# Kernel optimization log

Hardware: AMD Instinct MI355X
Metric: run time of the kernel (lower is better)

The kernel has to match this reference:

```python
import jax, jax.numpy as jnp
import numpy as np

D, H, W = 40, 32, 88
BEV_H, BEV_W = 125, 125
X_MIN, X_MAX, DX = -50.0, 50.0, 0.8
Y_MIN, Y_MAX, DY = -50.0, 50.0, 0.8
Z_MIN, DZ = -10.0, 20.0


def _voxel_indices():
    """Replicates frustum creation + get_geometry + index computation.
    Returns (flat_idx, valid) each of shape (D, H, W). Faithful to the
    original's sequential in-place max() semantics."""
    # depth_grid = arange(1, 41, 1) + 1  -> 2..41
    depth = jnp.arange(1.0, 41.0, 1.0) + 1.0            # (D,)
    xs = jnp.linspace(0.0, W - 1.0, W)                  # (W,)
    ys = jnp.linspace(0.0, H - 1.0, H)                  # (H,)
    d = depth[:, None, None]                            # (D,1,1)
    xd = jnp.broadcast_to(xs[None, None, :] * d, (D, H, W))  # x*depth
    yd = jnp.broadcast_to(ys[None, :, None] * d, (D, H, W))  # y*depth
    zd = jnp.broadcast_to(d, (D, H, W))                       # depth
    # first points_d.max(): over columns (xd, yd, zd)
    max1 = jnp.maximum(xd.max(), jnp.maximum(yd.max(), zd.max()))
    gx = xd / max1 * (X_MAX - X_MIN) + X_MIN
    # second points_d.max(): column 0 was overwritten in-place by gx
    max2 = jnp.maximum(gx.max(), jnp.maximum(yd.max(), zd.max()))
    gy = yd / max2 * (Y_MAX - Y_MIN) + Y_MIN
    gz = zd
    # voxelize (torch .long() truncates; all values here are >= 0)
    ix = ((gx - X_MIN) / DX).astype(jnp.int32)
    iy = ((gy - Y_MIN) / DY).astype(jnp.int32)
    iz = ((gz - Z_MIN) / DZ).astype(jnp.int32)
    valid = (ix >= 0) & (ix < BEV_W) & (iy >= 0) & (iy < BEV_H) & (iz >= 0)
    flat_idx = jnp.where(valid, iy * BEV_W + ix, 0)
    return flat_idx, valid


def setup_inputs() -> dict:
    key = jax.random.key(0)
    k1, k2, k3, k4, k5 = jax.random.split(key, 5)
    B, N, C = 1, 6, 128
    return {
        "img_feat": jax.random.normal(k1, (B, N, C, H, W), dtype=jnp.float32),
        "depth_logits": jax.random.normal(k2, (B, N, D, H, W), dtype=jnp.float32),
        "rots": jax.random.normal(k3, (B, N, 3, 3), dtype=jnp.float32),
        "trans": jax.random.normal(k4, (B, N, 3), dtype=jnp.float32),
        "intrins": jax.random.normal(k5, (B, N, 3, 3), dtype=jnp.float32),
    }


def reference(img_feat, depth_logits, rots, trans, intrins):
    B, N, C, h, w = img_feat.shape
    depth_probs = jax.nn.softmax(depth_logits, axis=2)         # (B,N,D,H,W)
    # depth-weighted outer product: (B,N,D,H,W,C)
    feats = jnp.einsum('bnchw,bndhw->bndhwc', img_feat, depth_probs)
    flat_feats = feats.reshape(-1, C)                          # (B*N*D*H*W, C)
    flat_idx, valid = _voxel_indices()                         # (D,H,W)
    idx = jnp.broadcast_to(flat_idx[None, None], (B, N, D, h, w)).reshape(-1)
    msk = jnp.broadcast_to(valid[None, None], (B, N, D, h, w)).reshape(-1)
    flat_feats = jnp.where(msk[:, None], flat_feats, 0.0)
    bev = jax.ops.segment_sum(flat_feats, idx, num_segments=BEV_H * BEV_W)
    bev = bev.reshape(BEV_H, BEV_W, C)
    return jnp.transpose(bev, (2, 0, 1))[None]                 # (1, C, 125, 125)
```

## Files before the change

kernel.cpp:

```cpp
#include <hip/hip_runtime.h>


constexpr int D = 40, H = 32, W = 88, HW = H * W;
constexpr int C = 128, NCAM = 6;
constexpr int BEV = 125, NBINS = BEV * BEV;
constexpr int NCOLS = NCAM * HW;
constexpr int LISTCAP = 192;

typedef __attribute__((ext_vector_type(8))) unsigned short us8;
typedef __attribute__((ext_vector_type(4))) float f4;

__device__ __forceinline__ unsigned short f2bf(float x) {
    unsigned u = __float_as_uint(x);
    return (unsigned short)((u + 0x7FFF + ((u >> 16) & 1)) >> 16);
}
__device__ __forceinline__ float b2f(unsigned short u) {
    return __uint_as_float(((unsigned)u) << 16);
}

struct Tabs { short XP[D][126]; short YP[D][126]; };
constexpr Tabs make_tabs() {
    Tabs t{};
    for (int d = 0; d < D; ++d) {
        int dep = d + 2;
        int cntx[126] = {};
        for (int w = 0; w < W; ++w) {
            float gx = (float)(w * dep) / 3567.0f * 100.0f - 50.0f;
            int ix = (int)((gx + 50.0f) / 0.8f);
            if (ix < 125) cntx[ix]++;
        }
        t.XP[d][0] = 0;
        for (int X = 0; X < 125; ++X) t.XP[d][X + 1] = (short)(t.XP[d][X] + cntx[X]);
        int cnty[126] = {};
        for (int h = 0; h < H; ++h) {
            float gy = (float)(h * dep) / 1271.0f * 100.0f - 50.0f;
            int iy = (int)((gy + 50.0f) / 0.8f);
            if (iy < 125) cnty[iy]++;
        }
        t.YP[d][0] = 0;
        for (int Y = 0; Y < 125; ++Y) t.YP[d][Y + 1] = (short)(t.YP[d][Y] + cnty[Y]);
    }
    return t;
}
__device__ const Tabs g_tab = make_tabs();

struct SegTable { unsigned a[4096]; unsigned b[4096]; int n; };

constexpr SegTable make_segs() {
    SegTable S{};
    Tabs t = make_tabs();
    int ns = 0;
    for (int iy = 0; iy < 125; ++iy) {
        int cnt[125] = {};
        for (int d = 0; d < D; ++d) {
            int yc = t.YP[d][iy + 1] - t.YP[d][iy];
            if (yc == 0) continue;
            for (int X = 0; X < 125; ++X)
                cnt[X] += (t.XP[d][X + 1] - t.XP[d][X]) * yc;
        }
        int X = 0;
        while (X < 125) {
            if (cnt[X] > 176) {
                int d0 = 0;
                while (d0 < D) {
                    int run = 0, d1 = d0;
                    while (d1 < D) {
                        int piece = (t.XP[d1][X + 1] - t.XP[d1][X]) *
                                    (t.YP[d1][iy + 1] - t.YP[d1][iy]);
                        if (d1 > d0 && run + piece > 128) break;
                        run += piece; ++d1;
                    }
                    if (run > 0) {
                        S.a[ns] = ((unsigned)iy << 16) | ((unsigned)X << 8) | (unsigned)(X + 1);
                        S.b[ns] = (1u << 31) | ((unsigned)d0 << 25) | ((unsigned)d1 << 19) | (unsigned)run;
                        ++ns;
                    }
                    d0 = d1;
                }
                ++X;
            } else {
                int X0 = X, run = 0;
                while (X < 125 && (X - X0) < 16 && cnt[X] <= 176 &&
                       (X == X0 || run + cnt[X] <= 128)) {
                    run += cnt[X]; ++X;
                }
                if (run > 0) {
                    S.a[ns] = ((unsigned)iy << 16) | ((unsigned)X0 << 8) | (unsigned)X;
                    S.b[ns] = ((unsigned)0 << 25) | ((unsigned)D << 19) | (unsigned)run;
                    ++ns;
                }
            }
        }
    }
    S.n = ns;
    return S;
}
constexpr SegTable g_ct = make_segs();
constexpr int NSEG = g_ct.n;
static_assert(NSEG > 0 && NSEG <= 4096, "seg table overflow");
__device__ const SegTable g_segs = g_ct;

constexpr int PACK_BLOCKS = (C / 8) * (HW / 32);
constexpr int SMAX_BLOCKS = NCOLS / 256;
constexpr int ZERO_TOTAL  = C * NBINS / 4;
constexpr int ZERO_BLOCKS = (ZERO_TOTAL + 1023) / 1024;
constexpr int MEGA_BLOCKS = PACK_BLOCKS + SMAX_BLOCKS + ZERO_BLOCKS;

__global__ void __launch_bounds__(256) mega_kernel(
        const float* __restrict__ feat,
        const float* __restrict__ logits,
        float* __restrict__ probs_t,
        unsigned short* __restrict__ feat_p,
        float* __restrict__ out) {
    __shared__ __align__(16) float tile[NCAM * 8 * 37];
    int b = blockIdx.x, t = threadIdx.x;

    if (b < PACK_BLOCKS) {
        int c0  = (b / 88) * 8;
        int hw0 = (b % 88) * 32;
        int cq = t >> 5, hwL = t & 31;
#pragma unroll
        for (int n = 0; n < NCAM; ++n)
            tile[(n * 8 + cq) * 37 + hwL] =
                feat[((size_t)(n * C + c0 + cq)) * HW + hw0 + hwL];
        __syncthreads();
        int hl = t >> 3, cL = t & 7;
        us8 v;
#pragma unroll
        for (int n = 0; n < NCAM; ++n)
            v[n] = f2bf(tile[(n * 8 + cL) * 37 + hl]);
        v[6] = 0; v[7] = 0;
        *(us8*)(feat_p + ((size_t)(hw0 + hl) * C + (c0 + cL)) * 8) = v;

    } else if (b < PACK_BLOCKS + SMAX_BLOCKS) {
        int col = (b - PACK_BLOCKS) * 256 + t;
        int n  = col / HW;
        int hw = col - n * HW;
        const float* src = logits + ((size_t)n * D) * HW + hw;
        float v[D];
        float m = -3.402823466e+38f;
#pragma unroll
        for (int d = 0; d < D; ++d) {
            v[d] = src[(size_t)d * HW];
            m = fmaxf(m, v[d]);
        }
        float s = 0.f;
#pragma unroll
        for (int d = 0; d < D; ++d) { v[d] = expf(v[d] - m); s += v[d]; }
        float inv = 1.0f / s;
#pragma unroll
        for (int d = 0; d < D; ++d)
            probs_t[(size_t)((d << 12) | hw) * 8 + n] = v[d] * inv;

    } else {
        int base = (b - PACK_BLOCKS - SMAX_BLOCKS) * 1024;
#pragma unroll
        for (int k = 0; k < 4; ++k) {
            int i = base + k * 256 + t;
            if (i < ZERO_TOTAL) ((f4*)out)[i] = f4{0.f, 0.f, 0.f, 0.f};
        }
    }
}

__global__ void __launch_bounds__(128, 8) gather_kernel(
        const unsigned short* __restrict__ feat_p,
        const float* __restrict__ probs_t,
        float* __restrict__ out) {
    __shared__ float T[2][16][66];
    __shared__ unsigned list[LISTCAP];
    int slot  = blockIdx.x >> 1;
    int chalf = blockIdx.x & 1;
    unsigned da = g_segs.a[slot], db = g_segs.b[slot];
    int iy = da >> 16, X0 = (da >> 8) & 0xFF, X1 = da & 0xFF;
    int width = X1 - X0;
    bool split = (db >> 31) != 0;
    int d0 = (db >> 25) & 0x3F, d1 = (db >> 19) & 0x3F;
    int P  = (int)(db & 0x7FFFF);
    int t = threadIdx.x;

    if (t < 64) {
        int d = d0 + t;
        if (d < d1) {
            int off = 0;
            for (int dd = d0; dd < d; ++dd)
                off += (g_tab.YP[dd][iy + 1] - g_tab.YP[dd][iy]) *
                       (g_tab.XP[dd][X1] - g_tab.XP[dd][X0]);
            int hb = g_tab.YP[d][iy], he = g_tab.YP[d][iy + 1];
            int p = off;
            for (int bl = 0; bl < width; ++bl) {
                int wb = g_tab.XP[d][X0 + bl], we = g_tab.XP[d][X0 + bl + 1];
                for (int h = hb; h < he; ++h)
                    for (int w = wb; w < we; ++w)
                        list[p++] = ((unsigned)bl << 18) | ((unsigned)d << 12)
                                  | (unsigned)(h * W + w);
            }
        }
    } else {
        float* Tf = &T[0][0][0];
        for (int i = t - 64; i < 2 * 16 * 66; i += 64) Tf[i] = 0.f;
    }
    __syncthreads();

    int lane = t & 63, dg = t >> 6;
    int c = chalf * 64 + lane;
    float* Tp = &T[dg][0][0];

    int npts = (P - dg + 1) >> 1;
    float racc = 0.f;
    int rbl = -1;
    for (int kb = 0; kb < npts; kb += 64) {
        int kidx = kb + lane;
        int myent = (int)list[min(dg + 2 * kidx, LISTCAP - 1)];
        int kk64 = min(64, npts - kb);
        for (int k0 = 0; k0 < kk64; k0 += 4) {
            int kk = min(4, kk64 - k0);
            unsigned pk[4]; us8 fv[4]; f4 pa[4], pb[4];
#pragma unroll
            for (int j = 0; j < 4; ++j) if (j < kk) {
                pk[j] = (unsigned)__shfl(myent, k0 + j);
                unsigned hw = pk[j] & 0xFFFu;
                fv[j] = *(const us8*)(feat_p + ((size_t)hw * C + (unsigned)c) * 8);
                const float* pp = probs_t + ((size_t)(pk[j] & 0x3FFFFu) << 3);
                pa[j] = *(const f4*)pp;
                pb[j] = *(const f4*)(pp + 4);
            }
#pragma unroll
            for (int j = 0; j < 4; ++j) if (j < kk) {
                float s = pa[j].x * b2f(fv[j][0]) + pa[j].y * b2f(fv[j][1])
                        + pa[j].z * b2f(fv[j][2]) + pa[j].w * b2f(fv[j][3])
                        + pb[j].x * b2f(fv[j][4]) + pb[j].y * b2f(fv[j][5]);
                int bl = (int)(pk[j] >> 18);
                if (bl != rbl) {
                    if (rbl >= 0) Tp[rbl * 66 + lane] += racc;
                    rbl = bl; racc = s;
                } else {
                    racc += s;
                }
            }
        }
    }
    if (rbl >= 0) Tp[rbl * 66 + lane] += racc;
    __syncthreads();

    int binbase = iy * BEV + X0;
#pragma unroll
    for (int it = 0; it < 8; ++it) {
        int bl = t & 15, cc = it * 8 + (t >> 4);
        if (bl < width) {
            float v = T[0][bl][cc] + T[1][bl][cc];
            float* dst = &out[(size_t)(chalf * 64 + cc) * NBINS + binbase + bl];
            if (split) atomicAdd(dst, v);
            else       *dst = v;
        }
    }
}

extern "C" void kernel_launch(void* const* d_in, const int* in_sizes, int n_in,
                              void* d_out, int out_size, void* d_ws, size_t ws_size,
                              hipStream_t stream) {
    const float* img_feat     = (const float*)d_in[0];
    const float* depth_logits = (const float*)d_in[1];
    float* out = (float*)d_out;

    char* p = (char*)d_ws;
    float*          probs_t = (float*)p;          p += (size_t)D * 4096 * 8 * 4;
    unsigned short* feat_p  = (unsigned short*)p; p += (size_t)HW * C * 8 * 2;

    mega_kernel<<<MEGA_BLOCKS, 256, 0, stream>>>(
        img_feat, depth_logits, probs_t, feat_p, out);
    gather_kernel<<<NSEG * 2, 128, 0, stream>>>(feat_p, probs_t, out);
}
```

Baseline: 125.4 us.

## Software-pipeline gather loads, prefetch list entries, and schedule heavy segments first

Replaces the batch-of-4 load-then-compute loop in the gather kernel with a double-buffered pipeline of three-entry groups. The next group's feature and probability loads are issued before the current group is consumed, and the next window's list entry is prefetched. Segments with large point counts are moved to the front of the table so long blocks start early and load imbalance at the tail shrinks. The launch bound drops from 8 to 4 waves per SIMD to leave registers for the extra buffers, at the cost of lower occupancy.

```diff
diff --git a/kernel.cpp b/kernel.cpp
--- a/kernel.cpp
+++ b/kernel.cpp
@@ -95,7 +95,19 @@
     S.n = ns;
     return S;
 }
-constexpr SegTable g_ct = make_segs();
+constexpr SegTable g_raw = make_segs();
+
+constexpr SegTable reorder_segs() {
+    SegTable R{};
+    int pos = 0;
+    for (int i = 0; i < g_raw.n; ++i)
+        if ((int)(g_raw.b[i] & 0x7FFFF) >= 120) { R.a[pos] = g_raw.a[i]; R.b[pos] = g_raw.b[i]; ++pos; }
+    for (int i = 0; i < g_raw.n; ++i)
+        if ((int)(g_raw.b[i] & 0x7FFFF) <  120) { R.a[pos] = g_raw.a[i]; R.b[pos] = g_raw.b[i]; ++pos; }
+    R.n = pos;
+    return R;
+}
+constexpr SegTable g_ct = reorder_segs();
 constexpr int NSEG = g_ct.n;
 static_assert(NSEG > 0 && NSEG <= 4096, "seg table overflow");
 __device__ const SegTable g_segs = g_ct;
@@ -162,7 +174,7 @@
     }
 }
 
-__global__ void __launch_bounds__(128, 8) gather_kernel(
+__global__ void __launch_bounds__(128, 4) gather_kernel(
         const unsigned short* __restrict__ feat_p,
         const float* __restrict__ probs_t,
         float* __restrict__ out) {
@@ -208,39 +220,54 @@
     int npts = (P - dg + 1) >> 1;
     float racc = 0.f;
     int rbl = -1;
+
+#define FETCH(I, BUF, P_)                                                     \
+    { pk##BUF[I] = (unsigned)__shfl(myent, (P_));                             \
+      fv##BUF[I] = *(const us8*)(feat_p +                                     \
+                    (((size_t)(pk##BUF[I] & 0xFFFu) * C + (unsigned)c) * 8)); \
+      const float* pp_ = probs_t + ((size_t)(pk##BUF[I] & 0x3FFFFu) << 3);    \
+      pa##BUF[I] = *(const f4*)pp_; pb##BUF[I] = *(const f4*)(pp_ + 4); }
+#define CONSUME(I, BUF)                                                       \
+    { float s_ = pa##BUF[I].x * b2f(fv##BUF[I][0]) + pa##BUF[I].y * b2f(fv##BUF[I][1]) \
+               + pa##BUF[I].z * b2f(fv##BUF[I][2]) + pa##BUF[I].w * b2f(fv##BUF[I][3]) \
+               + pb##BUF[I].x * b2f(fv##BUF[I][4]) + pb##BUF[I].y * b2f(fv##BUF[I][5]);\
+      int bl_ = (int)(pk##BUF[I] >> 18);                                      \
+      if (bl_ != rbl) { if (rbl >= 0) Tp[rbl * 66 + lane] += racc;            \
+                        rbl = bl_; racc = s_; }                               \
+      else racc += s_; }
+
+    int li0 = min(dg + 2 * lane, LISTCAP - 1);
+    int myent_next = (int)list[li0];
     for (int kb = 0; kb < npts; kb += 64) {
-        int kidx = kb + lane;
-        int myent = (int)list[min(dg + 2 * kidx, LISTCAP - 1)];
-        int kk64 = min(64, npts - kb);
-        for (int k0 = 0; k0 < kk64; k0 += 4) {
-            int kk = min(4, kk64 - k0);
-            unsigned pk[4]; us8 fv[4]; f4 pa[4], pb[4];
-#pragma unroll
-            for (int j = 0; j < 4; ++j) if (j < kk) {
-                pk[j] = (unsigned)__shfl(myent, k0 + j);
-                unsigned hw = pk[j] & 0xFFFu;
-                fv[j] = *(const us8*)(feat_p + ((size_t)hw * C + (unsigned)c) * 8);
-                const float* pp = probs_t + ((size_t)(pk[j] & 0x3FFFFu) << 3);
-                pa[j] = *(const f4*)pp;
-                pb[j] = *(const f4*)(pp + 4);
-            }
-#pragma unroll
-            for (int j = 0; j < 4; ++j) if (j < kk) {
-                float s = pa[j].x * b2f(fv[j][0]) + pa[j].y * b2f(fv[j][1])
-                        + pa[j].z * b2f(fv[j][2]) + pa[j].w * b2f(fv[j][3])
-                        + pb[j].x * b2f(fv[j][4]) + pb[j].y * b2f(fv[j][5]);
-                int bl = (int)(pk[j] >> 18);
-                if (bl != rbl) {
-                    if (rbl >= 0) Tp[rbl * 66 + lane] += racc;
-                    rbl = bl; racc = s;
-                } else {
-                    racc += s;
-                }
-            }
+        int myent = myent_next;
+        if (kb + 64 < npts) {
+            int li = min(dg + 2 * (kb + 64 + lane), LISTCAP - 1);
+            myent_next = (int)list[li];
+        }
+        int win = min(64, npts - kb);
+        unsigned pkA[3], pkB[3]; us8 fvA[3], fvB[3];
+        f4 paA[3], pbA[3], paB[3], pbB[3];
+#pragma unroll
+        for (int i = 0; i < 3; ++i) if (i < win) FETCH(i, A, i);
+        for (int j = 0; j < win; j += 6) {
+#pragma unroll
+            for (int i = 0; i < 3; ++i) { int p = j + 3 + i;
+                if (p < win) FETCH(i, B, p); }
+#pragma unroll
+            for (int i = 0; i < 3; ++i) { int p = j + i;
+                if (p < win) CONSUME(i, A); }
+#pragma unroll
+            for (int i = 0; i < 3; ++i) { int p = j + 6 + i;
+                if (p < win) FETCH(i, A, p); }
+#pragma unroll
+            for (int i = 0; i < 3; ++i) { int p = j + 3 + i;
+                if (p < win) CONSUME(i, B); }
         }
     }
     if (rbl >= 0) Tp[rbl * 66 + lane] += racc;
     __syncthreads();
+#undef FETCH
+#undef CONSUME
 
     int binbase = iy * BEV + X0;
 #pragma unroll
```

New measurement: 125.0 us. Within noise of the previous version (-0.3%).

## Precompute sorted point entry list in mega kernel and stream it in gather

Applied to the files above, without the earlier changes.

Adds a fill phase to the mega kernel that gives each frustum point its sorted position (bin-major, then depth) and writes a packed entry into a global entries array. Each segment gets a prefix start offset. The gather kernel then reads entries directly from global memory instead of building a per-block shared list serially with a few threads. The gather also remaps block IDs to spread work across XCDs, lowers the occupancy hint, and unrolls loads by 6. The cost is an extra global array, more mega-kernel work with a 40-iteration position loop per point, and a dependency on ix_of/iy_of matching the constexpr tables exactly.

```diff
diff --git a/kernel.cpp b/kernel.cpp
--- a/kernel.cpp
+++ b/kernel.cpp
@@ -4,8 +4,8 @@
 constexpr int D = 40, H = 32, W = 88, HW = H * W;
 constexpr int C = 128, NCAM = 6;
 constexpr int BEV = 125, NBINS = BEV * BEV;
+constexpr int NPTS = D * HW;
 constexpr int NCOLS = NCAM * HW;
-constexpr int LISTCAP = 192;
 
 typedef __attribute__((ext_vector_type(8))) unsigned short us8;
 typedef __attribute__((ext_vector_type(4))) float f4;
@@ -16,6 +16,15 @@
 }
 __device__ __forceinline__ float b2f(unsigned short u) {
     return __uint_as_float(((unsigned)u) << 16);
+}
+
+__device__ __forceinline__ int ix_of(int w, float dep) {
+    float gx = __fadd_rn(__fmul_rn(__fdiv_rn((float)w * dep, 3567.0f), 100.0f), -50.0f);
+    return (int)__fdiv_rn(__fadd_rn(gx, 50.0f), 0.8f);
+}
+__device__ __forceinline__ int iy_of(int h, float dep) {
+    float gy = __fadd_rn(__fmul_rn(__fdiv_rn((float)h * dep, 1271.0f), 100.0f), -50.0f);
+    return (int)__fdiv_rn(__fadd_rn(gy, 50.0f), 0.8f);
 }
 
 struct Tabs { short XP[D][126]; short YP[D][126]; };
@@ -44,12 +53,13 @@
 }
 __device__ const Tabs g_tab = make_tabs();
 
-struct SegTable { unsigned a[4096]; unsigned b[4096]; int n; };
+struct SegTable { unsigned a[4096]; unsigned b[4096]; unsigned start[4096]; int n; };
 
 constexpr SegTable make_segs() {
     SegTable S{};
     Tabs t = make_tabs();
     int ns = 0;
+    unsigned running = 0;
     for (int iy = 0; iy < 125; ++iy) {
         int cnt[125] = {};
         for (int d = 0; d < D; ++d) {
@@ -72,7 +82,8 @@
                     }
                     if (run > 0) {
                         S.a[ns] = ((unsigned)iy << 16) | ((unsigned)X << 8) | (unsigned)(X + 1);
-                        S.b[ns] = (1u << 31) | ((unsigned)d0 << 25) | ((unsigned)d1 << 19) | (unsigned)run;
+                        S.b[ns] = (1u << 31) | (unsigned)run;
+                        S.start[ns] = running; running += (unsigned)run;
                         ++ns;
                     }
                     d0 = d1;
@@ -86,7 +97,8 @@
                 }
                 if (run > 0) {
                     S.a[ns] = ((unsigned)iy << 16) | ((unsigned)X0 << 8) | (unsigned)X;
-                    S.b[ns] = ((unsigned)0 << 25) | ((unsigned)D << 19) | (unsigned)run;
+                    S.b[ns] = (unsigned)run;
+                    S.start[ns] = running; running += (unsigned)run;
                     ++ns;
                 }
             }
@@ -104,13 +116,15 @@
 constexpr int SMAX_BLOCKS = NCOLS / 256;
 constexpr int ZERO_TOTAL  = C * NBINS / 4;
 constexpr int ZERO_BLOCKS = (ZERO_TOTAL + 1023) / 1024;
-constexpr int MEGA_BLOCKS = PACK_BLOCKS + SMAX_BLOCKS + ZERO_BLOCKS;
+constexpr int FILL_BLOCKS = NPTS / 256;
+constexpr int MEGA_BLOCKS = PACK_BLOCKS + SMAX_BLOCKS + ZERO_BLOCKS + FILL_BLOCKS;
 
 __global__ void __launch_bounds__(256) mega_kernel(
         const float* __restrict__ feat,
         const float* __restrict__ logits,
         float* __restrict__ probs_t,
         unsigned short* __restrict__ feat_p,
+        unsigned* __restrict__ entries,
         float* __restrict__ out) {
     __shared__ __align__(16) float tile[NCAM * 8 * 37];
     int b = blockIdx.x, t = threadIdx.x;
@@ -152,97 +166,108 @@
         for (int d = 0; d < D; ++d)
             probs_t[(size_t)((d << 12) | hw) * 8 + n] = v[d] * inv;
 
-    } else {
+    } else if (b < PACK_BLOCKS + SMAX_BLOCKS + ZERO_BLOCKS) {
         int base = (b - PACK_BLOCKS - SMAX_BLOCKS) * 1024;
 #pragma unroll
         for (int k = 0; k < 4; ++k) {
             int i = base + k * 256 + t;
             if (i < ZERO_TOTAL) ((f4*)out)[i] = f4{0.f, 0.f, 0.f, 0.f};
         }
-    }
-}
-
-__global__ void __launch_bounds__(128, 8) gather_kernel(
+
+    } else {
+        int pt = (b - PACK_BLOCKS - SMAX_BLOCKS - ZERO_BLOCKS) * 256 + t;
+        int d = pt / HW, hw = pt - d * HW, h = hw / W, w = hw - h * W;
+        float dep = (float)(d + 2);
+        int X = ix_of(w, dep), Y = iy_of(h, dep);
+        if (X <= 124 && Y <= 124) {
+            int pos = 0;
+#pragma unroll 8
+            for (int dd = 0; dd < D; ++dd) {
+                int ypY = g_tab.YP[dd][Y];
+                int yc  = g_tab.YP[dd][Y + 1] - ypY;
+                int xpX = g_tab.XP[dd][X];
+                int xc  = g_tab.XP[dd][X + 1] - xpX;
+                pos += ypY * g_tab.XP[dd][125] + yc * xpX
+                     + ((dd < d) ? xc * yc : 0);
+            }
+            pos += (h - g_tab.YP[d][Y]) * (g_tab.XP[d][X + 1] - g_tab.XP[d][X])
+                 + (w - g_tab.XP[d][X]);
+            unsigned bin = (unsigned)(Y * BEV + X);
+            entries[pos] = (bin << 18) | ((unsigned)d << 12) | (unsigned)hw;
+        }
+    }
+}
+
+constexpr int GTOT = NSEG * 2;
+
+__global__ void __launch_bounds__(128, 4) gather_kernel(
         const unsigned short* __restrict__ feat_p,
         const float* __restrict__ probs_t,
+        const unsigned* __restrict__ entries,
         float* __restrict__ out) {
     __shared__ float T[2][16][66];
-    __shared__ unsigned list[LISTCAP];
-    int slot  = blockIdx.x >> 1;
-    int chalf = blockIdx.x & 1;
+    int u = (int)(blockIdx.x & 7) * ((GTOT + 7) / 8) + (int)(blockIdx.x >> 3);
+    if (u >= GTOT) return;
+    int slot = u >> 1, chalf = u & 1;
     unsigned da = g_segs.a[slot], db = g_segs.b[slot];
+    unsigned s0 = g_segs.start[slot];
     int iy = da >> 16, X0 = (da >> 8) & 0xFF, X1 = da & 0xFF;
     int width = X1 - X0;
     bool split = (db >> 31) != 0;
-    int d0 = (db >> 25) & 0x3F, d1 = (db >> 19) & 0x3F;
-    int P  = (int)(db & 0x7FFFF);
+    int P = (int)(db & 0x7FFFFFFF);
+    int binbase = iy * BEV + X0;
     int t = threadIdx.x;
-
-    if (t < 64) {
-        int d = d0 + t;
-        if (d < d1) {
-            int off = 0;
-            for (int dd = d0; dd < d; ++dd)
-                off += (g_tab.YP[dd][iy + 1] - g_tab.YP[dd][iy]) *
-                       (g_tab.XP[dd][X1] - g_tab.XP[dd][X0]);
-            int hb = g_tab.YP[d][iy], he = g_tab.YP[d][iy + 1];
-            int p = off;
-            for (int bl = 0; bl < width; ++bl) {
-                int wb = g_tab.XP[d][X0 + bl], we = g_tab.XP[d][X0 + bl + 1];
-                for (int h = hb; h < he; ++h)
-                    for (int w = wb; w < we; ++w)
-                        list[p++] = ((unsigned)bl << 18) | ((unsigned)d << 12)
-                                  | (unsigned)(h * W + w);
-            }
-        }
-    } else {
-        float* Tf = &T[0][0][0];
-        for (int i = t - 64; i < 2 * 16 * 66; i += 64) Tf[i] = 0.f;
-    }
-    __syncthreads();
-
     int lane = t & 63, dg = t >> 6;
-    int c = chalf * 64 + lane;
     float* Tp = &T[dg][0][0];
 
-    int npts = (P - dg + 1) >> 1;
+    for (int i = lane; i < 16 * 66; i += 64) Tp[i] = 0.f;
+
+    int half = (P + 1) >> 1;
+    int beg = (int)s0 + (dg ? half : 0);
+    int end = (int)s0 + (dg ? P : half);
+
     float racc = 0.f;
     int rbl = -1;
-    for (int kb = 0; kb < npts; kb += 64) {
-        int kidx = kb + lane;
-        int myent = (int)list[min(dg + 2 * kidx, LISTCAP - 1)];
-        int kk64 = min(64, npts - kb);
-        for (int k0 = 0; k0 < kk64; k0 += 4) {
-            int kk = min(4, kk64 - k0);
-            unsigned pk[4]; us8 fv[4]; f4 pa[4], pb[4];
-#pragma unroll
-            for (int j = 0; j < 4; ++j) if (j < kk) {
-                pk[j] = (unsigned)__shfl(myent, k0 + j);
-                unsigned hw = pk[j] & 0xFFFu;
-                fv[j] = *(const us8*)(feat_p + ((size_t)hw * C + (unsigned)c) * 8);
-                const float* pp = probs_t + ((size_t)(pk[j] & 0x3FFFFu) << 3);
-                pa[j] = *(const f4*)pp;
-                pb[j] = *(const f4*)(pp + 4);
-            }
-#pragma unroll
-            for (int j = 0; j < 4; ++j) if (j < kk) {
-                float s = pa[j].x * b2f(fv[j][0]) + pa[j].y * b2f(fv[j][1])
-                        + pa[j].z * b2f(fv[j][2]) + pa[j].w * b2f(fv[j][3])
-                        + pb[j].x * b2f(fv[j][4]) + pb[j].y * b2f(fv[j][5]);
-                int bl = (int)(pk[j] >> 18);
-                if (bl != rbl) {
-                    if (rbl >= 0) Tp[rbl * 66 + lane] += racc;
-                    rbl = bl; racc = s;
-                } else {
-                    racc += s;
-                }
-            }
-        }
+    int i = beg;
+    for (; i + 6 <= end; i += 6) {
+        unsigned pk[6];
+#pragma unroll
+        for (int j = 0; j < 6; ++j) pk[j] = entries[i + j];
+        us8 fv[6];
+#pragma unroll
+        for (int j = 0; j < 6; ++j)
+            fv[j] = *(const us8*)(feat_p +
+                     (((size_t)(pk[j] & 0xFFFu) * C + (unsigned)(chalf * 64 + lane)) * 8));
+#pragma unroll
+        for (int j = 0; j < 6; ++j) {
+            const float* pp = probs_t + ((size_t)(pk[j] & 0x3FFFFu) << 3);
+            float s = ((pp[0] * b2f(fv[j][0]) + pp[1] * b2f(fv[j][1]))
+                     + (pp[2] * b2f(fv[j][2]) + pp[3] * b2f(fv[j][3])))
+                     + (pp[4] * b2f(fv[j][4]) + pp[5] * b2f(fv[j][5]));
+            int bl = (int)(pk[j] >> 18) - binbase;
+            if (bl != rbl) {
+                if (rbl >= 0) Tp[rbl * 66 + lane] += racc;
+                rbl = bl; racc = s;
+            } else racc += s;
+        }
+    }
+    for (; i < end; ++i) {
+        unsigned pk = entries[i];
+        us8 fv = *(const us8*)(feat_p +
+                  (((size_t)(pk & 0xFFFu) * C + (unsigned)(chalf * 64 + lane)) * 8));
+        const float* pp = probs_t + ((size_t)(pk & 0x3FFFFu) << 3);
+        float s = ((pp[0] * b2f(fv[0]) + pp[1] * b2f(fv[1]))
+                 + (pp[2] * b2f(fv[2]) + pp[3] * b2f(fv[3])))
+                 + (pp[4] * b2f(fv[4]) + pp[5] * b2f(fv[5]));
+        int bl = (int)(pk >> 18) - binbase;
+        if (bl != rbl) {
+            if (rbl >= 0) Tp[rbl * 66 + lane] += racc;
+            rbl = bl; racc = s;
+        } else racc += s;
     }
     if (rbl >= 0) Tp[rbl * 66 + lane] += racc;
     __syncthreads();
 
-    int binbase = iy * BEV + X0;
 #pragma unroll
     for (int it = 0; it < 8; ++it) {
         int bl = t & 15, cc = it * 8 + (t >> 4);
@@ -265,8 +290,9 @@
     char* p = (char*)d_ws;
     float*          probs_t = (float*)p;          p += (size_t)D * 4096 * 8 * 4;
     unsigned short* feat_p  = (unsigned short*)p; p += (size_t)HW * C * 8 * 2;
+    unsigned*       entries = (unsigned*)p;       p += (size_t)NPTS * 4;
 
     mega_kernel<<<MEGA_BLOCKS, 256, 0, stream>>>(
-        img_feat, depth_logits, probs_t, feat_p, out);
-    gather_kernel<<<NSEG * 2, 128, 0, stream>>>(feat_p, probs_t, out);
-}
+        img_feat, depth_logits, probs_t, feat_p, entries, out);
+    gather_kernel<<<((GTOT + 7) / 8) * 8, 128, 0, stream>>>(feat_p, probs_t, entries, out);
+}
```

Result: slower. 131.0 us (+4.5%).
